# Kernel tuning notes

Measured on AMD Instinct MI355X. Metric: run time of the kernel, lower is better.

## Reference

```python
import jax, jax.numpy as jnp
import numpy as np
import math

EMBED_DIM = 512
NUM_HEADS = 8
BLOCK_SIZE = 16
RANK = 32
B, N = 1, 4096
HEAD_DIM = EMBED_DIM // NUM_HEADS
SCALE = math.sqrt(HEAD_DIM)  # note: the torch module MULTIPLIES q by sqrt(head_dim)


def _block_causal_mask(n, block):
    # block-diagonal lower-triangular mask, identical for every head
    idx = jnp.arange(n)
    same_block = (idx[:, None] // block) == (idx[None, :] // block)
    causal = idx[:, None] >= idx[None, :]
    return (same_block & causal).astype(jnp.float32)  # [N, N]


def setup_inputs() -> dict:
    key = jax.random.key(0)
    ks = jax.random.split(key, 12)
    s = 0.02
    C, R = EMBED_DIM, RANK
    return {
        "x": jax.random.normal(ks[0], (B, N, C), dtype=jnp.float32),
        # low-rank query proj: Linear(C->R) then Linear(R->C); torch weight is [out, in]
        "q_w1": jax.random.normal(ks[1], (R, C), dtype=jnp.float32) * s,
        "q_w2": jax.random.normal(ks[2], (C, R), dtype=jnp.float32) * s,
        # key_value: Linear(C->2R) then Linear(2R->2C)
        "kv_w1": jax.random.normal(ks[3], (2 * R, C), dtype=jnp.float32) * s,
        "kv_w2": jax.random.normal(ks[4], (2 * C, 2 * R), dtype=jnp.float32) * s,
        # dynamic_focus: depthwise 1x1 conv (per-channel scale+bias) then pointwise 1x1 conv
        "dw_w": jax.random.normal(ks[5], (C,), dtype=jnp.float32) * s,
        "dw_b": jax.random.normal(ks[6], (C,), dtype=jnp.float32) * s,
        "pw_w": jax.random.normal(ks[7], (C, C), dtype=jnp.float32) * s,
        "pw_b": jax.random.normal(ks[8], (C,), dtype=jnp.float32) * s,
        # output proj: Linear(C->R) then Linear(R->C)
        "p_w1": jax.random.normal(ks[9], (R, C), dtype=jnp.float32) * s,
        "p_w2": jax.random.normal(ks[10], (C, R), dtype=jnp.float32) * s,
    }


def reference(x, q_w1, q_w2, kv_w1, kv_w2, dw_w, dw_b, pw_w, pw_b, p_w1, p_w2):
    Bv, Nv, C = x.shape
    H, D = NUM_HEADS, HEAD_DIM

    # low-rank q / kv projections (no bias)
    q = (x @ q_w1.T) @ q_w2.T                              # [B, N, C]
    kv = (x @ kv_w1.T) @ kv_w2.T                           # [B, N, 2C]

    q = q.reshape(Bv, Nv, H, D).transpose(0, 2, 1, 3)      # [B, H, N, D]
    kv = kv.reshape(Bv, Nv, 2, H, D).transpose(2, 0, 3, 1, 4)
    k, v = kv[0], kv[1]                                    # [B, H, N, D]

    q = q * SCALE
    attn = jnp.einsum("bhnd,bhmd->bhnm", q, k)             # [B, H, N, N]
    # faithful to source: full-row softmax FIRST, then block-diag causal mask
    mask = _block_causal_mask(Nv, BLOCK_SIZE)              # [N, N]
    attn = jax.nn.softmax(attn, axis=-1) * mask

    wv = jnp.einsum("bhnm,bhmd->bhnd", attn, v)            # [B, H, N, D]
    wv = wv.transpose(0, 2, 1, 3).reshape(Bv, Nv, C)       # [B, N, C]

    # dynamic_focus: depthwise 1x1 conv == per-channel affine; pointwise 1x1 conv == linear.
    # Spatial reshape to (sqrt(N), sqrt(N)) is a no-op for 1x1 convs, so stay in [B, N, C].
    dyn = wv * dw_w + dw_b
    dyn = dyn @ pw_w.T + pw_b

    y = dyn + x
    y = (y @ p_w1.T) @ p_w2.T
    return y
```

## Files before the change

kernel.cpp:

```cpp
#include <hip/hip_runtime.h>

#define NFULL 4096
#define CDIM  512
#define HEADS 8
#define DDIM  64

typedef unsigned short u16;
typedef short bf16x8 __attribute__((ext_vector_type(8)));
typedef float f32x4 __attribute__((ext_vector_type(4)));

#if __has_builtin(__builtin_amdgcn_exp2f)
__device__ __forceinline__ float exp2_hw(float x) { return __builtin_amdgcn_exp2f(x); }
#else
__device__ __forceinline__ float exp2_hw(float x) {
  float r;
  asm volatile("v_exp_f32 %0, %1\n\ts_nop 1" : "=v"(r) : "v"(x));
  return r;
}
#endif
#define EXP2(x) exp2_hw(x)

#define QSCALE 11.541560327111707f

__device__ __forceinline__ float dot4(float4 a, float4 b) {
  return a.x * b.x + a.y * b.y + a.z * b.z + a.w * b.w;
}

__device__ __forceinline__ u16 f2bf(float x) {
  union { float f; unsigned u; } v; v.f = x;
  unsigned r = v.u + 0x7fffu + ((v.u >> 16) & 1u);
  return (u16)(r >> 16);
}

__device__ __forceinline__ float bf2f(u16 b) {
  union { unsigned u; float f; } v; v.u = ((unsigned)b) << 16;
  return v.f;
}

__global__ __launch_bounds__(256) void k_pre(const float* __restrict__ x,
                                             const float* __restrict__ qw1,
                                             const float* __restrict__ kvw1,
                                             u16* __restrict__ t_bf,
                                             const float* __restrict__ pww,
                                             const float* __restrict__ dww,
                                             const float* __restrict__ dwb,
                                             const float* __restrict__ pwb,
                                             const float* __restrict__ pw1,
                                             const float* __restrict__ pw2,
                                             float* __restrict__ bias2,
                                             u16* __restrict__ pwbf,
                                             u16* __restrict__ pw1bf,
                                             u16* __restrict__ pw2bf) {
  __shared__ __align__(16) u16 Xs[32][72];
  __shared__ __align__(16) u16 Ws[96][72];
  const int tid = threadIdx.x;

  if (blockIdx.x >= 128) {
    const int b = blockIdx.x - 128;
    if (b < 2) {
      const int c = b * 256 + tid;
      float acc = 0.f;
      for (int e = 0; e < 512; e += 4)
        acc += dot4(*(const float4*)&pww[(size_t)c * 512 + e], *(const float4*)&dwb[e]);
      bias2[c] = acc + pwb[c];
    } else {
      const float* src;
      u16* dst;
      bool scale = false;
      int base;
      if (b < 66)      { base = (b - 2) * 4096 + tid * 16;  src = pww; dst = pwbf; scale = true; }
      else if (b < 70) { base = (b - 66) * 4096 + tid * 16; src = pw1; dst = pw1bf; }
      else             { base = (b - 70) * 4096 + tid * 16; src = pw2; dst = pw2bf; }
      const int e0 = base & 511;
      u16 o[16];
#pragma unroll
      for (int q = 0; q < 4; ++q) {
        float4 w = *(const float4*)&src[base + q * 4];
        if (scale) {
          const float4 d = *(const float4*)&dww[e0 + q * 4];
          w.x *= d.x; w.y *= d.y; w.z *= d.z; w.w *= d.w;
        }
        o[q * 4 + 0] = f2bf(w.x); o[q * 4 + 1] = f2bf(w.y);
        o[q * 4 + 2] = f2bf(w.z); o[q * 4 + 3] = f2bf(w.w);
      }
      *(uint4*)&dst[base] = *(const uint4*)&o[0];
      *(uint4*)&dst[base + 8] = *(const uint4*)&o[8];
    }
    return;
  }

  const int r0 = blockIdx.x * 32;
  const int wave = tid >> 6, lane = tid & 63;
  const int lrow = lane & 15, g = lane >> 4;
  const int rs = wave >> 1, ws2 = wave & 1;

  f32x4 acc[3];
#pragma unroll
  for (int sub = 0; sub < 3; ++sub) acc[sub] = (f32x4){0.f, 0.f, 0.f, 0.f};

  for (int k0 = 0; k0 < 512; k0 += 64) {
    __syncthreads();
    {
      const int row = tid >> 3, c16 = (tid & 7) * 8;
      const float* __restrict__ src = x + (size_t)(r0 + row) * 512 + k0 + c16;
      const float4 v0 = *(const float4*)(src);
      const float4 v1 = *(const float4*)(src + 4);
      u16 tmp[8] = {f2bf(v0.x), f2bf(v0.y), f2bf(v0.z), f2bf(v0.w),
                    f2bf(v1.x), f2bf(v1.y), f2bf(v1.z), f2bf(v1.w)};
      *(uint4*)&Xs[row][c16] = *(const uint4*)&tmp[0];
    }
    for (int u = tid; u < 768; u += 256) {
      const int c = u >> 3, c16 = (u & 7) * 8;
      const float* __restrict__ src =
          (c < 32 ? qw1 + (size_t)c * 512 : kvw1 + (size_t)(c - 32) * 512) + k0 + c16;
      const float4 v0 = *(const float4*)(src);
      const float4 v1 = *(const float4*)(src + 4);
      u16 tmp[8] = {f2bf(v0.x), f2bf(v0.y), f2bf(v0.z), f2bf(v0.w),
                    f2bf(v1.x), f2bf(v1.y), f2bf(v1.z), f2bf(v1.w)};
      *(uint4*)&Ws[c][c16] = *(const uint4*)&tmp[0];
    }
    __syncthreads();
    const bf16x8 a0 = *(const bf16x8*)&Xs[rs * 16 + lrow][g * 8];
    const bf16x8 a1 = *(const bf16x8*)&Xs[rs * 16 + lrow][32 + g * 8];
#pragma unroll
    for (int sub = 0; sub < 3; ++sub) {
      const int c = (ws2 * 3 + sub) * 16 + lrow;
      const bf16x8 b0 = *(const bf16x8*)&Ws[c][g * 8];
      const bf16x8 b1 = *(const bf16x8*)&Ws[c][32 + g * 8];
      acc[sub] = __builtin_amdgcn_mfma_f32_16x16x32_bf16(b0, a0, acc[sub], 0, 0, 0);
      acc[sub] = __builtin_amdgcn_mfma_f32_16x16x32_bf16(b1, a1, acc[sub], 0, 0, 0);
    }
  }
  const int n = r0 + rs * 16 + lrow;
#pragma unroll
  for (int sub = 0; sub < 3; ++sub) {
    u16 o4[4] = {f2bf(acc[sub][0]), f2bf(acc[sub][1]),
                 f2bf(acc[sub][2]), f2bf(acc[sub][3])};
    *(uint2*)&t_bf[(size_t)n * 96 + (ws2 * 3 + sub) * 16 + g * 4] = *(const uint2*)o4;
  }
}

__global__ __launch_bounds__(256) void k_proj2(const u16* __restrict__ t_bf,
                                               const float* __restrict__ qw2,
                                               const float* __restrict__ kvw2,
                                               u16* __restrict__ qb,
                                               u16* __restrict__ kb,
                                               float* __restrict__ vh) {
  __shared__ __align__(16) u16 Ts[64][72];
  __shared__ __align__(16) u16 Wsh[128][72];
  const int cb = blockIdx.x % 12;
  const int r0 = (blockIdx.x / 12) * 64;
  const int tid = threadIdx.x;
  const int wave = tid >> 6, lane = tid & 63;
  const int lrow = lane & 15, g = lane >> 4;
  const bool isq = cb < 4;
  const int c0 = isq ? cb * 128 : 512 + (cb - 4) * 128;

  for (int u = tid; u < 512; u += 256) {
    const int row = u >> 3, ch = (u & 7) * 8;
    uint4 v = {0u, 0u, 0u, 0u};
    if (isq) {
      if (ch < 32) v = *(const uint4*)&t_bf[(size_t)(r0 + row) * 96 + ch];
    } else {
      v = *(const uint4*)&t_bf[(size_t)(r0 + row) * 96 + 32 + ch];
    }
    *(uint4*)&Ts[row][ch] = v;
  }
  if (isq) {
    for (int u = tid; u < 1024; u += 256) {
      const int col = u >> 3, cf = (u & 7) * 4;
      const float4 v = *(const float4*)&qw2[(size_t)(c0 + col) * 32 + cf];
      u16 tmp[4] = {f2bf(v.x), f2bf(v.y), f2bf(v.z), f2bf(v.w)};
      *(uint2*)&Wsh[col][cf] = *(const uint2*)&tmp[0];
    }
  } else {
    for (int u = tid; u < 2048; u += 256) {
      const int col = u >> 4, cf = (u & 15) * 4;
      const float4 v = *(const float4*)&kvw2[(size_t)(c0 - 512 + col) * 64 + cf];
      u16 tmp[4] = {f2bf(v.x), f2bf(v.y), f2bf(v.z), f2bf(v.w)};
      *(uint2*)&Wsh[col][cf] = *(const uint2*)&tmp[0];
    }
  }
  __syncthreads();

  const int n = r0 + wave * 16 + lrow;
  if (isq) {
    const bf16x8 aq = *(const bf16x8*)&Ts[wave * 16 + lrow][g * 8];
#pragma unroll
    for (int sub = 0; sub < 8; ++sub) {
      const bf16x8 b0 = *(const bf16x8*)&Wsh[sub * 16 + lrow][g * 8];
      f32x4 acc = {0.f, 0.f, 0.f, 0.f};
      acc = __builtin_amdgcn_mfma_f32_16x16x32_bf16(b0, aq, acc, 0, 0, 0);
      const int colg0 = c0 + sub * 16 + g * 4;
      const int hh = colg0 >> 6, d0 = colg0 & 63;
      u16 o4[4] = {f2bf(acc[0] * QSCALE), f2bf(acc[1] * QSCALE),
                   f2bf(acc[2] * QSCALE), f2bf(acc[3] * QSCALE)};
      *(uint2*)&qb[((size_t)hh * NFULL + n) * 64 + d0] = *(const uint2*)o4;
    }
  } else {
    const bf16x8 a0 = *(const bf16x8*)&Ts[wave * 16 + lrow][g * 8];
    const bf16x8 a1 = *(const bf16x8*)&Ts[wave * 16 + lrow][32 + g * 8];
#pragma unroll
    for (int sub = 0; sub < 8; ++sub) {
      const bf16x8 b0 = *(const bf16x8*)&Wsh[sub * 16 + lrow][g * 8];
      const bf16x8 b1 = *(const bf16x8*)&Wsh[sub * 16 + lrow][32 + g * 8];
      f32x4 acc = {0.f, 0.f, 0.f, 0.f};
      acc = __builtin_amdgcn_mfma_f32_16x16x32_bf16(b0, a0, acc, 0, 0, 0);
      acc = __builtin_amdgcn_mfma_f32_16x16x32_bf16(b1, a1, acc, 0, 0, 0);
      const int colg0 = c0 + sub * 16 + g * 4;
      if (colg0 < 1024) {
        const int c2 = colg0 - 512;
        const int hh = c2 >> 6, d0 = c2 & 63;
        u16 o4[4] = {f2bf(acc[0]), f2bf(acc[1]), f2bf(acc[2]), f2bf(acc[3])};
        *(uint2*)&kb[((size_t)hh * NFULL + n) * 64 + d0] = *(const uint2*)o4;
      } else {
        const int c2 = colg0 - 1024;
        const int hh = c2 >> 6, d0 = c2 & 63;
        float4 o4;
        o4.x = acc[0]; o4.y = acc[1]; o4.z = acc[2]; o4.w = acc[3];
        *(float4*)&vh[((size_t)hh * NFULL + n) * 64 + d0] = o4;
      }
    }
  }
}

__global__ __launch_bounds__(256, 2) void k_attn(const u16* __restrict__ qb,
                                                 const u16* __restrict__ kb,
                                                 const float* __restrict__ vh,
                                                 u16* __restrict__ wv16,
                                                 float* __restrict__ dsp) {
  __shared__ __align__(16) u16 KB[4][64][64];
  __shared__ float P_lds[8][16][17];
  __shared__ float Ds[4][8][16];

  const int h = blockIdx.x & 7;
  const int qt = (blockIdx.x >> 3) & 31;
  const int s = blockIdx.x >> 8;
  const int q0 = qt * 128;
  const int tid = threadIdx.x;
  const int wave = tid >> 6, lane = tid & 63;
  const int lrow = lane & 15, g = lane >> 4;

  const u16* __restrict__ Qg = qb + ((size_t)h * NFULL + q0) * 64;
  const u16* __restrict__ Kg = kb + ((size_t)h * NFULL + (size_t)s * 2048) * 64;

  bf16x8 qf[8][2];
#pragma unroll
  for (int j = 0; j < 8; ++j) {
    qf[j][0] = *(const bf16x8*)&Qg[(j * 16 + lrow) * 64 + g * 8];
    qf[j][1] = *(const bf16x8*)&Qg[(j * 16 + lrow) * 64 + 32 + g * 8];
  }

  const int srow8 = lane >> 3;
  const int scol = ((lane & 7) ^ srow8) << 3;

#define STAGE(T, B)                                                           \
  do {                                                                        \
    const u16* tb_ = Kg + (size_t)(T) * 64 * 64;                              \
    {                                                                         \
      const u16* src_ = tb_ + (wave * 16 + srow8) * 64 + scol;                \
      u16* dst_ = &KB[(B)][wave * 16][0];                                     \
      __builtin_amdgcn_global_load_lds(                                       \
          (const __attribute__((address_space(1))) unsigned*)src_,            \
          (__attribute__((address_space(3))) unsigned*)dst_, 16, 0, 0);       \
    }                                                                         \
    {                                                                         \
      const u16* src_ = tb_ + (wave * 16 + 8 + srow8) * 64 + scol;            \
      u16* dst_ = &KB[(B)][wave * 16][0] + 512;                               \
      __builtin_amdgcn_global_load_lds(                                       \
          (const __attribute__((address_space(1))) unsigned*)src_,            \
          (__attribute__((address_space(3))) unsigned*)dst_, 16, 0, 0);       \
    }                                                                         \
  } while (0)

  const int rsw = wave * 16 + lrow;
  const int x0 = (g ^ (lrow & 7)) * 8;
  const int x1 = ((g + 4) ^ (lrow & 7)) * 8;

  float dsum[8];
#pragma unroll
  for (int j = 0; j < 8; ++j) dsum[j] = 0.f;
  const bool dg = (s == (qt >> 4));
  const int ql = qt & 15;

  auto tile = [&](int t, int b) {
    const bf16x8 kf0 = *(const bf16x8*)&KB[b][rsw][x0];
    const bf16x8 kf1 = *(const bf16x8*)&KB[b][rsw][x1];
#pragma unroll
    for (int hs = 0; hs < 2; ++hs) {
      f32x4 a[4];
      __builtin_amdgcn_s_setprio(1);
#pragma unroll
      for (int f = 0; f < 4; ++f) {
        f32x4 t4 = {0.f, 0.f, 0.f, 0.f};
        t4 = __builtin_amdgcn_mfma_f32_16x16x32_bf16(kf0, qf[hs * 4 + f][0], t4, 0, 0, 0);
        t4 = __builtin_amdgcn_mfma_f32_16x16x32_bf16(kf1, qf[hs * 4 + f][1], t4, 0, 0, 0);
        a[f] = t4;
      }
      __builtin_amdgcn_s_setprio(0);
      const bool isd = dg && (t == ql * 2 + hs);
#pragma unroll
      for (int f = 0; f < 4; ++f) {
        const float e0 = EXP2(a[f][0]);
        const float e1 = EXP2(a[f][1]);
        const float e2 = EXP2(a[f][2]);
        const float e3 = EXP2(a[f][3]);
        dsum[hs * 4 + f] += (e0 + e1) + (e2 + e3);
        if (isd && f == wave) {
          const int rr = g * 4;
          const int J = hs * 4 + wave;
          P_lds[J][rr + 0][lrow] = (rr + 0 <= lrow) ? e0 : 0.f;
          P_lds[J][rr + 1][lrow] = (rr + 1 <= lrow) ? e1 : 0.f;
          P_lds[J][rr + 2][lrow] = (rr + 2 <= lrow) ? e2 : 0.f;
          P_lds[J][rr + 3][lrow] = (rr + 3 <= lrow) ? e3 : 0.f;
        }
      }
    }
  };

  STAGE(0, 0); STAGE(1, 1); STAGE(2, 2);

  for (int t = 0; t < 28; t += 2) {
    STAGE(t + 3, (t + 3) & 3);
    asm volatile("s_waitcnt vmcnt(6)" ::: "memory");
    tile(t, t & 3);
    STAGE(t + 4, (t + 4) & 3);
    asm volatile("s_waitcnt vmcnt(6)" ::: "memory");
    tile(t + 1, (t + 1) & 3);
  }
  STAGE(31, 3);
  asm volatile("s_waitcnt vmcnt(6)" ::: "memory");
  tile(28, 0);
  asm volatile("s_waitcnt vmcnt(4)" ::: "memory");
  tile(29, 1);
  asm volatile("s_waitcnt vmcnt(2)" ::: "memory");
  tile(30, 2);
  asm volatile("s_waitcnt vmcnt(0)" ::: "memory");
  tile(31, 3);
#undef STAGE

#pragma unroll
  for (int j = 0; j < 8; ++j) {
    dsum[j] += __shfl_xor(dsum[j], 16);
    dsum[j] += __shfl_xor(dsum[j], 32);
  }
  if (g == 0) {
#pragma unroll
    for (int j = 0; j < 8; ++j) Ds[wave][j][lrow] = dsum[j];
  }
  __syncthreads();

  if (tid < 128) {
    const int J2 = tid >> 4, r = tid & 15;
    const float den = Ds[0][J2][r] + Ds[1][J2][r] + Ds[2][J2][r] + Ds[3][J2][r];
    dsp[((size_t)s * HEADS + h) * NFULL + q0 + J2 * 16 + r] = den;
  }

  if (dg) {
#pragma unroll
    for (int m = 0; m < 2; ++m) {
      const int J = m * 4 + wave;
      const float* __restrict__ V =
          vh + ((size_t)h * NFULL + q0 + J * 16) * 64 + g * 16;
      float o[16];
#pragma unroll
      for (int dd = 0; dd < 16; ++dd) o[dd] = 0.f;
#pragma unroll
      for (int k = 0; k < 16; ++k) {
        const float p = P_lds[J][k][lrow];
        const float4 v0 = *(const float4*)&V[k * 64 + 0];
        const float4 v1 = *(const float4*)&V[k * 64 + 4];
        const float4 v2 = *(const float4*)&V[k * 64 + 8];
        const float4 v3 = *(const float4*)&V[k * 64 + 12];
        o[0] += p * v0.x;  o[1] += p * v0.y;  o[2] += p * v0.z;  o[3] += p * v0.w;
        o[4] += p * v1.x;  o[5] += p * v1.y;  o[6] += p * v1.z;  o[7] += p * v1.w;
        o[8] += p * v2.x;  o[9] += p * v2.y;  o[10] += p * v2.z; o[11] += p * v2.w;
        o[12] += p * v3.x; o[13] += p * v3.y; o[14] += p * v3.z; o[15] += p * v3.w;
      }
      u16 ob[16];
#pragma unroll
      for (int dd = 0; dd < 16; ++dd) ob[dd] = f2bf(o[dd]);
      u16* __restrict__ op =
          wv16 + (size_t)(q0 + J * 16 + lrow) * CDIM + h * 64 + g * 16;
      *(uint4*)&op[0] = *(const uint4*)&ob[0];
      *(uint4*)&op[8] = *(const uint4*)&ob[8];
    }
  }
}

__global__ __launch_bounds__(256) void k_dyn(const u16* __restrict__ wv16,
                                             const float* __restrict__ x,
                                             const u16* __restrict__ pwbf,
                                             const float* __restrict__ bias2,
                                             const float* __restrict__ dsp,
                                             u16* __restrict__ y16) {
  __shared__ __align__(16) u16 Ab[64][72];
  __shared__ __align__(16) u16 Wb[64][72];
  const int rb = blockIdx.x >> 3, cb = blockIdx.x & 7;
  const int r0 = rb * 64, c0 = cb * 64;
  const int tid = threadIdx.x;
  const int wave = tid >> 6, lane = tid & 63;
  const int lrow = lane & 15, g = lane >> 4;
  const int srow = tid >> 2;
  const int skc = (tid & 3) * 16;

  float inv8[8];
#pragma unroll
  for (int hh = 0; hh < 8; ++hh) {
    const size_t base = (size_t)hh * NFULL + r0 + srow;
    inv8[hh] = 1.0f / (dsp[base] + dsp[(size_t)8 * NFULL + base]);
  }

  f32x4 acc[4];
#pragma unroll
  for (int ct = 0; ct < 4; ++ct) acc[ct] = (f32x4){0.f, 0.f, 0.f, 0.f};

  const u16* __restrict__ ap = wv16 + (size_t)(r0 + srow) * 512 + skc;
  const u16* __restrict__ wp = pwbf + (size_t)(c0 + srow) * 512 + skc;
  uint4 av0 = *(const uint4*)ap;
  uint4 av1 = *(const uint4*)(ap + 8);
  uint4 w0 = *(const uint4*)wp;
  uint4 w1 = *(const uint4*)(wp + 8);

  for (int k0 = 0; k0 < 512; k0 += 64) {
    const float sc = inv8[k0 >> 6];
    u16 ab16[16];
    const u16* pa0 = (const u16*)&av0;
    const u16* pa1 = (const u16*)&av1;
#pragma unroll
    for (int e = 0; e < 8; ++e) ab16[e] = f2bf(bf2f(pa0[e]) * sc);
#pragma unroll
    for (int e = 0; e < 8; ++e) ab16[8 + e] = f2bf(bf2f(pa1[e]) * sc);
    __syncthreads();
    *(uint4*)&Ab[srow][skc] = *(const uint4*)&ab16[0];
    *(uint4*)&Ab[srow][skc + 8] = *(const uint4*)&ab16[8];
    *(uint4*)&Wb[srow][skc] = w0;
    *(uint4*)&Wb[srow][skc + 8] = w1;
    __syncthreads();
    if (k0 + 64 < 512) {
      av0 = *(const uint4*)(ap + k0 + 64);
      av1 = *(const uint4*)(ap + k0 + 64 + 8);
      w0 = *(const uint4*)(wp + k0 + 64);
      w1 = *(const uint4*)(wp + k0 + 64 + 8);
    }
#pragma unroll
    for (int kk = 0; kk < 2; ++kk) {
      const bf16x8 af = *(const bf16x8*)&Ab[wave * 16 + lrow][kk * 32 + g * 8];
#pragma unroll
      for (int ct = 0; ct < 4; ++ct) {
        const bf16x8 wf = *(const bf16x8*)&Wb[ct * 16 + lrow][kk * 32 + g * 8];
        acc[ct] = __builtin_amdgcn_mfma_f32_16x16x32_bf16(wf, af, acc[ct], 0, 0, 0);
      }
    }
  }
  const int row = r0 + wave * 16 + lrow;
#pragma unroll
  for (int ct = 0; ct < 4; ++ct) {
    const int c = c0 + ct * 16 + g * 4;
    const float4 bb = *(const float4*)&bias2[c];
    const float4 xv = *(const float4*)&x[(size_t)row * 512 + c];
    u16 o4[4];
    o4[0] = f2bf(acc[ct][0] + bb.x + xv.x);
    o4[1] = f2bf(acc[ct][1] + bb.y + xv.y);
    o4[2] = f2bf(acc[ct][2] + bb.z + xv.z);
    o4[3] = f2bf(acc[ct][3] + bb.w + xv.w);
    *(uint2*)&y16[(size_t)row * 512 + c] = *(const uint2*)o4;
  }
}

__global__ __launch_bounds__(256) void k_pout(const u16* __restrict__ y16,
                                              const u16* __restrict__ pw1bf,
                                              const u16* __restrict__ pw2bf,
                                              float* __restrict__ out) {
  __shared__ __align__(16) u16 yb[16][520];
  __shared__ float tp_part[2][32][17];
  const int r0 = (blockIdx.x >> 1) * 16;
  const int chalf = blockIdx.x & 1;
  const int tid = threadIdx.x;
  const int wave = tid >> 6, lane = tid & 63;
  const int lrow = lane & 15, g = lane >> 4;

  for (int rep = 0; rep < 4; ++rep) {
    const int idx = rep * 256 + tid;
    const int row = idx >> 6, c8 = (idx & 63) * 8;
    *(uint4*)&yb[row][c8] = *(const uint4*)&y16[(size_t)(r0 + row) * 512 + c8];
  }
  __syncthreads();

  {
    const int ct1 = wave & 1, kh = wave >> 1;
    f32x4 acc = {0.f, 0.f, 0.f, 0.f};
#pragma unroll
    for (int ks = 0; ks < 8; ++ks) {
      const int K = kh * 256 + ks * 32 + g * 8;
      const bf16x8 aw = *(const bf16x8*)&pw1bf[(size_t)(ct1 * 16 + lrow) * 512 + K];
      const bf16x8 bf = *(const bf16x8*)&yb[lrow][K];
      acc = __builtin_amdgcn_mfma_f32_16x16x32_bf16(aw, bf, acc, 0, 0, 0);
    }
#pragma unroll
    for (int j = 0; j < 4; ++j)
      tp_part[kh][ct1 * 16 + g * 4 + j][lrow] = acc[j];
  }
  __syncthreads();

  union { u16 a[8]; bf16x8 v; } bq;
#pragma unroll
  for (int i = 0; i < 8; ++i) {
    const int k = g * 8 + i;
    bq.a[i] = f2bf(tp_part[0][k][lrow] + tp_part[1][k][lrow]);
  }

#pragma unroll
  for (int t = 0; t < 4; ++t) {
    const int ct = chalf * 16 + wave * 4 + t;
    const bf16x8 aw = *(const bf16x8*)&pw2bf[(size_t)(ct * 16 + lrow) * 32 + g * 8];
    f32x4 acc = {0.f, 0.f, 0.f, 0.f};
    acc = __builtin_amdgcn_mfma_f32_16x16x32_bf16(aw, bq.v, acc, 0, 0, 0);
    float4 res;
    res.x = acc[0]; res.y = acc[1]; res.z = acc[2]; res.w = acc[3];
    *(float4*)&out[(size_t)(r0 + lrow) * 512 + ct * 16 + g * 4] = res;
  }
}

extern "C" void kernel_launch(void* const* d_in, const int* in_sizes, int n_in,
                              void* d_out, int out_size, void* d_ws, size_t ws_size,
                              hipStream_t stream) {
  const float* x     = (const float*)d_in[0];
  const float* q_w1  = (const float*)d_in[1];
  const float* q_w2  = (const float*)d_in[2];
  const float* kv_w1 = (const float*)d_in[3];
  const float* kv_w2 = (const float*)d_in[4];
  const float* dw_w  = (const float*)d_in[5];
  const float* dw_b  = (const float*)d_in[6];
  const float* pw_w  = (const float*)d_in[7];
  const float* pw_b  = (const float*)d_in[8];
  const float* p_w1  = (const float*)d_in[9];
  const float* p_w2  = (const float*)d_in[10];
  float* out = (float*)d_out;

  char* ws = (char*)d_ws;
  float* dsp   = (float*)ws;
  float* bias2 = (float*)(ws + 262144);
  u16*   pwbf  = (u16*)(ws + 262144 + 4096);
  u16*   pw1bf = pwbf + 262144;
  u16*   pw2bf = pw1bf + 16384;
  u16*   t_bf  = pw2bf + 16384;
  u16*   qbw   = t_bf + (size_t)NFULL * 96;
  u16*   kbw   = qbw + (size_t)HEADS * NFULL * DDIM;
  float* vh    = (float*)(kbw + (size_t)HEADS * NFULL * DDIM);
  u16*   wv16  = (u16*)(vh + (size_t)HEADS * NFULL * DDIM);
  u16*   y16   = qbw;

  k_pre<<<202, 256, 0, stream>>>(x, q_w1, kv_w1, t_bf, pw_w, dw_w, dw_b, pw_b,
                                 p_w1, p_w2, bias2, pwbf, pw1bf, pw2bf);
  k_proj2<<<(NFULL / 64) * 12, 256, 0, stream>>>(t_bf, q_w2, kv_w2, qbw, kbw, vh);
  k_attn<<<2 * HEADS * (NFULL / 128), 256, 0, stream>>>(qbw, kbw, vh, wv16, dsp);
  k_dyn<<<(NFULL / 64) * 8, 256, 0, stream>>>(wv16, x, pwbf, bias2, dsp, y16);
  k_pout<<<(NFULL / 16) * 2, 256, 0, stream>>>(y16, pw1bf, pw2bf, out);
}
```

Baseline: 83.30 us.

## Fold pointwise conv weights into low-rank output projection and fuse dyn with pout

```diff
diff --git a/kernel.cpp b/kernel.cpp
--- a/kernel.cpp
+++ b/kernel.cpp
@@ -48,7 +48,7 @@
                                              const float* __restrict__ pw1,
                                              const float* __restrict__ pw2,
                                              float* __restrict__ bias2,
-                                             u16* __restrict__ pwbf,
+                                             u16* __restrict__ wcbf,
                                              u16* __restrict__ pw1bf,
                                              u16* __restrict__ pw2bf) {
   __shared__ __align__(16) u16 Xs[32][72];
@@ -63,23 +63,29 @@
       for (int e = 0; e < 512; e += 4)
         acc += dot4(*(const float4*)&pww[(size_t)c * 512 + e], *(const float4*)&dwb[e]);
       bias2[c] = acc + pwb[c];
+    } else if (b < 66) {
+      const int b2 = b - 2;
+      const int r = b2 >> 1;
+      const int k = (b2 & 1) * 256 + tid;
+      float acc = 0.f;
+      for (int c = 0; c < 512; c += 4) {
+        const float4 p = *(const float4*)&pw1[(size_t)r * 512 + c];
+        acc += p.x * pww[(size_t)(c + 0) * 512 + k];
+        acc += p.y * pww[(size_t)(c + 1) * 512 + k];
+        acc += p.z * pww[(size_t)(c + 2) * 512 + k];
+        acc += p.w * pww[(size_t)(c + 3) * 512 + k];
+      }
+      wcbf[(size_t)r * 512 + k] = f2bf(acc * dww[k]);
     } else {
       const float* src;
       u16* dst;
-      bool scale = false;
       int base;
-      if (b < 66)      { base = (b - 2) * 4096 + tid * 16;  src = pww; dst = pwbf; scale = true; }
-      else if (b < 70) { base = (b - 66) * 4096 + tid * 16; src = pw1; dst = pw1bf; }
-      else             { base = (b - 70) * 4096 + tid * 16; src = pw2; dst = pw2bf; }
-      const int e0 = base & 511;
+      if (b < 70) { base = (b - 66) * 4096 + tid * 16; src = pw1; dst = pw1bf; }
+      else        { base = (b - 70) * 4096 + tid * 16; src = pw2; dst = pw2bf; }
       u16 o[16];
 #pragma unroll
       for (int q = 0; q < 4; ++q) {
-        float4 w = *(const float4*)&src[base + q * 4];
-        if (scale) {
-          const float4 d = *(const float4*)&dww[e0 + q * 4];
-          w.x *= d.x; w.y *= d.y; w.z *= d.z; w.w *= d.w;
-        }
+        const float4 w = *(const float4*)&src[base + q * 4];
         o[q * 4 + 0] = f2bf(w.x); o[q * 4 + 1] = f2bf(w.y);
         o[q * 4 + 2] = f2bf(w.z); o[q * 4 + 3] = f2bf(w.w);
       }
@@ -143,14 +149,35 @@
 __global__ __launch_bounds__(256) void k_proj2(const u16* __restrict__ t_bf,
                                                const float* __restrict__ qw2,
                                                const float* __restrict__ kvw2,
+                                               const float* __restrict__ pw1,
+                                               const float* __restrict__ bias2,
                                                u16* __restrict__ qb,
                                                u16* __restrict__ kb,
-                                               float* __restrict__ vh) {
+                                               float* __restrict__ vh,
+                                               float* __restrict__ bias_c) {
   __shared__ __align__(16) u16 Ts[64][72];
   __shared__ __align__(16) u16 Wsh[128][72];
+  __shared__ float red[8][32];
+  const int tid = threadIdx.x;
+
+  if (blockIdx.x >= 768) {
+    const int r = tid & 31, part = tid >> 5;
+    float acc = 0.f;
+    for (int c = part * 64; c < part * 64 + 64; ++c)
+      acc += bias2[c] * pw1[(size_t)r * 512 + c];
+    red[part][r] = acc;
+    __syncthreads();
+    if (tid < 32) {
+      float s = 0.f;
+#pragma unroll
+      for (int p = 0; p < 8; ++p) s += red[p][tid];
+      bias_c[tid] = s;
+    }
+    return;
+  }
+
   const int cb = blockIdx.x % 12;
   const int r0 = (blockIdx.x / 12) * 64;
-  const int tid = threadIdx.x;
   const int wave = tid >> 6, lane = tid & 63;
   const int lrow = lane & 15, g = lane >> 4;
   const bool isq = cb < 4;
@@ -388,118 +415,67 @@
   }
 }
 
-__global__ __launch_bounds__(256) void k_dyn(const u16* __restrict__ wv16,
+__global__ __launch_bounds__(256) void k_out(const u16* __restrict__ wv16,
                                              const float* __restrict__ x,
-                                             const u16* __restrict__ pwbf,
-                                             const float* __restrict__ bias2,
                                              const float* __restrict__ dsp,
-                                             u16* __restrict__ y16) {
-  __shared__ __align__(16) u16 Ab[64][72];
-  __shared__ __align__(16) u16 Wb[64][72];
-  const int rb = blockIdx.x >> 3, cb = blockIdx.x & 7;
-  const int r0 = rb * 64, c0 = cb * 64;
+                                             const u16* __restrict__ wcbf,
+                                             const u16* __restrict__ pw1bf,
+                                             const u16* __restrict__ pw2bf,
+                                             const float* __restrict__ bias_c,
+                                             float* __restrict__ out) {
+  __shared__ __align__(16) u16 wvb[16][520];
+  __shared__ __align__(16) u16 xb[16][520];
+  __shared__ float tp_part[4][32][17];
+  __shared__ float invs[16][8];
+  const int r0 = blockIdx.x * 16;
   const int tid = threadIdx.x;
   const int wave = tid >> 6, lane = tid & 63;
   const int lrow = lane & 15, g = lane >> 4;
-  const int srow = tid >> 2;
-  const int skc = (tid & 3) * 16;
-
-  float inv8[8];
-#pragma unroll
-  for (int hh = 0; hh < 8; ++hh) {
-    const size_t base = (size_t)hh * NFULL + r0 + srow;
-    inv8[hh] = 1.0f / (dsp[base] + dsp[(size_t)8 * NFULL + base]);
-  }
-
-  f32x4 acc[4];
-#pragma unroll
-  for (int ct = 0; ct < 4; ++ct) acc[ct] = (f32x4){0.f, 0.f, 0.f, 0.f};
-
-  const u16* __restrict__ ap = wv16 + (size_t)(r0 + srow) * 512 + skc;
-  const u16* __restrict__ wp = pwbf + (size_t)(c0 + srow) * 512 + skc;
-  uint4 av0 = *(const uint4*)ap;
-  uint4 av1 = *(const uint4*)(ap + 8);
-  uint4 w0 = *(const uint4*)wp;
-  uint4 w1 = *(const uint4*)(wp + 8);
-
-  for (int k0 = 0; k0 < 512; k0 += 64) {
-    const float sc = inv8[k0 >> 6];
-    u16 ab16[16];
-    const u16* pa0 = (const u16*)&av0;
-    const u16* pa1 = (const u16*)&av1;
-#pragma unroll
-    for (int e = 0; e < 8; ++e) ab16[e] = f2bf(bf2f(pa0[e]) * sc);
-#pragma unroll
-    for (int e = 0; e < 8; ++e) ab16[8 + e] = f2bf(bf2f(pa1[e]) * sc);
-    __syncthreads();
-    *(uint4*)&Ab[srow][skc] = *(const uint4*)&ab16[0];
-    *(uint4*)&Ab[srow][skc + 8] = *(const uint4*)&ab16[8];
-    *(uint4*)&Wb[srow][skc] = w0;
-    *(uint4*)&Wb[srow][skc + 8] = w1;
-    __syncthreads();
-    if (k0 + 64 < 512) {
-      av0 = *(const uint4*)(ap + k0 + 64);
-      av1 = *(const uint4*)(ap + k0 + 64 + 8);
-      w0 = *(const uint4*)(wp + k0 + 64);
-      w1 = *(const uint4*)(wp + k0 + 64 + 8);
-    }
-#pragma unroll
-    for (int kk = 0; kk < 2; ++kk) {
-      const bf16x8 af = *(const bf16x8*)&Ab[wave * 16 + lrow][kk * 32 + g * 8];
-#pragma unroll
-      for (int ct = 0; ct < 4; ++ct) {
-        const bf16x8 wf = *(const bf16x8*)&Wb[ct * 16 + lrow][kk * 32 + g * 8];
-        acc[ct] = __builtin_amdgcn_mfma_f32_16x16x32_bf16(wf, af, acc[ct], 0, 0, 0);
-      }
-    }
-  }
-  const int row = r0 + wave * 16 + lrow;
-#pragma unroll
-  for (int ct = 0; ct < 4; ++ct) {
-    const int c = c0 + ct * 16 + g * 4;
-    const float4 bb = *(const float4*)&bias2[c];
-    const float4 xv = *(const float4*)&x[(size_t)row * 512 + c];
-    u16 o4[4];
-    o4[0] = f2bf(acc[ct][0] + bb.x + xv.x);
-    o4[1] = f2bf(acc[ct][1] + bb.y + xv.y);
-    o4[2] = f2bf(acc[ct][2] + bb.z + xv.z);
-    o4[3] = f2bf(acc[ct][3] + bb.w + xv.w);
-    *(uint2*)&y16[(size_t)row * 512 + c] = *(const uint2*)o4;
-  }
-}
-
-__global__ __launch_bounds__(256) void k_pout(const u16* __restrict__ y16,
-                                              const u16* __restrict__ pw1bf,
-                                              const u16* __restrict__ pw2bf,
-                                              float* __restrict__ out) {
-  __shared__ __align__(16) u16 yb[16][520];
-  __shared__ float tp_part[2][32][17];
-  const int r0 = (blockIdx.x >> 1) * 16;
-  const int chalf = blockIdx.x & 1;
-  const int tid = threadIdx.x;
-  const int wave = tid >> 6, lane = tid & 63;
-  const int lrow = lane & 15, g = lane >> 4;
+
+  if (tid < 128) {
+    const int n = tid >> 3, hh = tid & 7;
+    const size_t base = (size_t)hh * NFULL + r0 + n;
+    invs[n][hh] = 1.0f / (dsp[base] + dsp[(size_t)8 * NFULL + base]);
+  }
+  __syncthreads();
 
   for (int rep = 0; rep < 4; ++rep) {
     const int idx = rep * 256 + tid;
     const int row = idx >> 6, c8 = (idx & 63) * 8;
-    *(uint4*)&yb[row][c8] = *(const uint4*)&y16[(size_t)(r0 + row) * 512 + c8];
+    const float sc = invs[row][c8 >> 6];
+    const uint4 wv8 = *(const uint4*)&wv16[(size_t)(r0 + row) * 512 + c8];
+    const u16* pw = (const u16*)&wv8;
+    u16 t8[8];
+#pragma unroll
+    for (int i = 0; i < 8; ++i) t8[i] = f2bf(bf2f(pw[i]) * sc);
+    *(uint4*)&wvb[row][c8] = *(const uint4*)&t8[0];
+    const float4 x0 = *(const float4*)&x[(size_t)(r0 + row) * 512 + c8];
+    const float4 x1 = *(const float4*)&x[(size_t)(r0 + row) * 512 + c8 + 4];
+    u16 u8[8] = {f2bf(x0.x), f2bf(x0.y), f2bf(x0.z), f2bf(x0.w),
+                 f2bf(x1.x), f2bf(x1.y), f2bf(x1.z), f2bf(x1.w)};
+    *(uint4*)&xb[row][c8] = *(const uint4*)&u8[0];
   }
   __syncthreads();
 
   {
-    const int ct1 = wave & 1, kh = wave >> 1;
-    f32x4 acc = {0.f, 0.f, 0.f, 0.f};
-#pragma unroll
-    for (int ks = 0; ks < 8; ++ks) {
-      const int K = kh * 256 + ks * 32 + g * 8;
-      const bf16x8 aw = *(const bf16x8*)&pw1bf[(size_t)(ct1 * 16 + lrow) * 512 + K];
-      const bf16x8 bf = *(const bf16x8*)&yb[lrow][K];
-      acc = __builtin_amdgcn_mfma_f32_16x16x32_bf16(aw, bf, acc, 0, 0, 0);
-    }
-#pragma unroll
-    for (int j = 0; j < 4; ++j)
-      tp_part[kh][ct1 * 16 + g * 4 + j][lrow] = acc[j];
+    const bool isx = (wave & 2) != 0;
+    const int kh = wave & 1;
+    const u16* __restrict__ Wsrc = isx ? pw1bf : wcbf;
+#pragma unroll
+    for (int rt = 0; rt < 2; ++rt) {
+      f32x4 acc = {0.f, 0.f, 0.f, 0.f};
+#pragma unroll
+      for (int ks = 0; ks < 8; ++ks) {
+        const int K = kh * 256 + ks * 32 + g * 8;
+        const bf16x8 aw = *(const bf16x8*)&Wsrc[(size_t)(rt * 16 + lrow) * 512 + K];
+        const bf16x8 bf = isx ? *(const bf16x8*)&xb[lrow][K]
+                              : *(const bf16x8*)&wvb[lrow][K];
+        acc = __builtin_amdgcn_mfma_f32_16x16x32_bf16(aw, bf, acc, 0, 0, 0);
+      }
+#pragma unroll
+      for (int j = 0; j < 4; ++j)
+        tp_part[wave][rt * 16 + g * 4 + j][lrow] = acc[j];
+    }
   }
   __syncthreads();
 
@@ -507,12 +483,13 @@
 #pragma unroll
   for (int i = 0; i < 8; ++i) {
     const int k = g * 8 + i;
-    bq.a[i] = f2bf(tp_part[0][k][lrow] + tp_part[1][k][lrow]);
-  }
-
-#pragma unroll
-  for (int t = 0; t < 4; ++t) {
-    const int ct = chalf * 16 + wave * 4 + t;
+    bq.a[i] = f2bf(tp_part[0][k][lrow] + tp_part[1][k][lrow] +
+                   tp_part[2][k][lrow] + tp_part[3][k][lrow] + bias_c[k]);
+  }
+
+#pragma unroll
+  for (int t = 0; t < 8; ++t) {
+    const int ct = wave * 8 + t;
     const bf16x8 aw = *(const bf16x8*)&pw2bf[(size_t)(ct * 16 + lrow) * 32 + g * 8];
     f32x4 acc = {0.f, 0.f, 0.f, 0.f};
     acc = __builtin_amdgcn_mfma_f32_16x16x32_bf16(aw, bq.v, acc, 0, 0, 0);
@@ -539,22 +516,23 @@
   float* out = (float*)d_out;
 
   char* ws = (char*)d_ws;
-  float* dsp   = (float*)ws;
-  float* bias2 = (float*)(ws + 262144);
-  u16*   pwbf  = (u16*)(ws + 262144 + 4096);
-  u16*   pw1bf = pwbf + 262144;
-  u16*   pw2bf = pw1bf + 16384;
-  u16*   t_bf  = pw2bf + 16384;
-  u16*   qbw   = t_bf + (size_t)NFULL * 96;
-  u16*   kbw   = qbw + (size_t)HEADS * NFULL * DDIM;
-  float* vh    = (float*)(kbw + (size_t)HEADS * NFULL * DDIM);
-  u16*   wv16  = (u16*)(vh + (size_t)HEADS * NFULL * DDIM);
-  u16*   y16   = qbw;
+  float* dsp    = (float*)ws;
+  float* bias2  = (float*)(ws + 262144);
+  float* bias_c = (float*)(ws + 262144 + 4096);
+  u16*   wcbf   = (u16*)(ws + 262144 + 8192);
+  u16*   pw1bf  = wcbf + 16384;
+  u16*   pw2bf  = pw1bf + 16384;
+  u16*   t_bf   = pw2bf + 16384;
+  u16*   qbw    = t_bf + (size_t)NFULL * 96;
+  u16*   kbw    = qbw + (size_t)HEADS * NFULL * DDIM;
+  float* vh     = (float*)(kbw + (size_t)HEADS * NFULL * DDIM);
+  u16*   wv16   = (u16*)(vh + (size_t)HEADS * NFULL * DDIM);
 
   k_pre<<<202, 256, 0, stream>>>(x, q_w1, kv_w1, t_bf, pw_w, dw_w, dw_b, pw_b,
-                                 p_w1, p_w2, bias2, pwbf, pw1bf, pw2bf);
-  k_proj2<<<(NFULL / 64) * 12, 256, 0, stream>>>(t_bf, q_w2, kv_w2, qbw, kbw, vh);
+                                 p_w1, p_w2, bias2, wcbf, pw1bf, pw2bf);
+  k_proj2<<<769, 256, 0, stream>>>(t_bf, q_w2, kv_w2, p_w1, bias2, qbw, kbw, vh,
+                                   bias_c);
   k_attn<<<2 * HEADS * (NFULL / 128), 256, 0, stream>>>(qbw, kbw, vh, wv16, dsp);
-  k_dyn<<<(NFULL / 64) * 8, 256, 0, stream>>>(wv16, x, pwbf, bias2, dsp, y16);
-  k_pout<<<(NFULL / 16) * 2, 256, 0, stream>>>(y16, pw1bf, pw2bf, out);
-}
+  k_out<<<NFULL / 16, 256, 0, stream>>>(wv16, x, dsp, wcbf, pw1bf, pw2bf, bias_c,
+                                        out);
+}
```

Result: faster. 75.24 us (-9.7%).
